# Kernel tuning notes

Hardware: AMD Instinct MI355X
Metric: run time of the kernel (lower is better)

Reference implementation:

```python
import jax, jax.numpy as jnp
import numpy as np

N = 2048      # nodes
E = 65536     # edges (avg degree 32)
D_I = 64      # input feature dim
D_O = 64      # output feature dim
EPS = 1e-6


def _one_hot_incidence(key, n, e):
    # each edge column has a single 1 at its endpoint node row -> [N, E]
    idx = jax.random.randint(key, (e,), 0, n)
    return jnp.zeros((n, e), jnp.float32).at[idx, jnp.arange(e)].set(1.0)


def setup_inputs() -> dict:
    key = jax.random.key(0)
    k_x, k_s, k_t, k_wf, k_ww = jax.random.split(key, 5)
    x = jax.random.normal(k_x, (N, D_I), jnp.float32)
    src = _one_hot_incidence(k_s, N, E)
    tgt = _one_hot_incidence(k_t, N, E)
    # xavier-uniform init for Linear(2*d_i, d_o) and Linear(2*d_i, 1)
    lim_f = float(np.sqrt(6.0 / (2 * D_I + D_O)))
    lim_w = float(np.sqrt(6.0 / (2 * D_I + 1)))
    W_f = jax.random.uniform(k_wf, (2 * D_I, D_O), jnp.float32, -lim_f, lim_f)
    b_f = jnp.zeros((D_O,), jnp.float32)
    W_w = jax.random.uniform(k_ww, (2 * D_I, 1), jnp.float32, -lim_w, lim_w)
    b_w = jnp.zeros((1,), jnp.float32)
    return {"x": x, "src": src, "tgt": tgt,
            "W_f": W_f, "b_f": b_f, "W_w": W_w, "b_w": b_w}


def reference(x, src, tgt, W_f, b_f, W_w, b_w):
    # gather source/target node features per edge via dense one-hot matmuls
    hsrc = src.T @ x                      # [E, d_i]
    htgt = tgt.T @ x                      # [E, d_i]
    h = jnp.concatenate([hsrc, htgt], axis=1)   # [E, 2*d_i]
    y = jax.nn.relu(h @ W_f + b_f)        # [E, d_o]
    a = h @ W_w + b_w                     # [E, 1]
    a_max = jnp.mean(a, axis=0, keepdims=True)
    a_exp = jnp.exp(a - a_max)            # [E, 1]
    a_sum = tgt @ a_exp                   # [N, 1] segment-sum over edges per target node
    a_tgt = tgt.T @ a_sum                 # [E, 1] broadcast denominators back to edges
    a_att = a_exp / (a_tgt + EPS)         # edge softmax weights
    o = tgt @ (y * a_att)                 # [N, d_o] weighted scatter-sum
    return o
```

## Files before the change

kernel.cpp:

```cpp
#include <hip/hip_runtime.h>
#include <hip/hip_bf16.h>

#define N_NODES 2048
#define N_EDGES 65536
#define D_IN    64
#define D_OUT   64
#define GAT_EPS 1e-6f

typedef unsigned short u16;
typedef unsigned int   u32;
typedef __attribute__((ext_vector_type(8))) short frag8;
typedef __attribute__((ext_vector_type(4))) float f32x4;

__device__ __forceinline__ u16 f2bf(float f) {
    union { u32 u; float f; } x; x.f = f;
    u32 lsb = (x.u >> 16) & 1u;
    x.u += 0x7fffu + lsb;
    return (u16)(x.u >> 16);
}

__global__ void k_extract(const uint4* __restrict__ src, const uint4* __restrict__ tgt,
                          int* __restrict__ sidx, int* __restrict__ tidx,
                          float* __restrict__ zero_base) {
    u32 b = blockIdx.x, tid = threadIdx.x;
    if (b < 520u) {
        u32 zi = b * 256u + tid;
        if (zi < 133120u) zero_base[zi] = 0.0f;
    }
    const uint4* m; int* idx;
    if (b < 2048u) { m = src; idx = sidx; }
    else           { m = tgt; idx = tidx; b -= 2048u; }
    u32 t0 = b * 256u + tid;
    const u32 S = 524288u;
    #pragma unroll 4
    for (u32 it = 0; it < 64u; ++it) {
        u32 t = t0 + it * S;
        uint4 v = m[t];
        if (v.x | v.y | v.z | v.w) {
            u32 elem = t * 4u;
            int n = (int)(elem >> 16);
            int e = (int)(elem & 65535u);
            if (v.x) idx[e]     = n;
            if (v.y) idx[e + 1] = n;
            if (v.z) idx[e + 2] = n;
            if (v.w) idx[e + 3] = n;
        }
    }
}

__global__ void __launch_bounds__(256) k_fused(
        const float* __restrict__ x,
        const int* __restrict__ sidx, const int* __restrict__ tidx,
        const float* __restrict__ Wf, const float* __restrict__ bf,
        const float* __restrict__ Ww, const float* __restrict__ bw,
        float* __restrict__ a_sum, float* __restrict__ out_acc) {
    __shared__ u16 wt[D_OUT * 2 * D_IN];
    __shared__ float ww[2 * D_IN];
    int tid = threadIdx.x;
    if (tid < 2 * D_IN) ww[tid] = Ww[tid];
    for (int i = tid; i < 2 * D_IN * D_OUT; i += 256) {
        int k = i >> 6, d = i & 63;
        wt[d * 128 + k] = f2bf(Wf[i]);
    }
    __syncthreads();

    int wave = tid >> 6, lane = tid & 63;
    int q = lane >> 4, r = lane & 15;
    int e0 = blockIdx.x * 64 + wave * 16;

    int s_r = sidx[e0 + r] & (N_NODES - 1);
    int t_r = tidx[e0 + r] & (N_NODES - 1);
    const float* xs = x + s_r * D_IN;
    const float* xt = x + t_r * D_IN;

    frag8 afr[4];
    float part = 0.0f;
    #pragma unroll
    for (int c = 0; c < 4; ++c) {
        const float* base = (c < 2 ? xs : xt) + (c & 1) * 32 + q * 8;
        int kb = (c >> 1) * 64 + (c & 1) * 32 + q * 8;
        float4 lo = *(const float4*)(base);
        float4 hi = *(const float4*)(base + 4);
        part += lo.x * ww[kb]     + lo.y * ww[kb + 1]
              + lo.z * ww[kb + 2] + lo.w * ww[kb + 3]
              + hi.x * ww[kb + 4] + hi.y * ww[kb + 5]
              + hi.z * ww[kb + 6] + hi.w * ww[kb + 7];
        frag8 f;
        f[0] = (short)f2bf(lo.x); f[1] = (short)f2bf(lo.y);
        f[2] = (short)f2bf(lo.z); f[3] = (short)f2bf(lo.w);
        f[4] = (short)f2bf(hi.x); f[5] = (short)f2bf(hi.y);
        f[6] = (short)f2bf(hi.z); f[7] = (short)f2bf(hi.w);
        afr[c] = f;
    }
    part += __shfl_xor(part, 16);
    part += __shfl_xor(part, 32);
    float ae = expf(part + bw[0]);
    if (lane < 16) atomicAdd(&a_sum[t_r], ae);

    f32x4 acc[4] = { {0,0,0,0}, {0,0,0,0}, {0,0,0,0}, {0,0,0,0} };
    #pragma unroll
    for (int c = 0; c < 4; ++c) {
        #pragma unroll
        for (int dt = 0; dt < 4; ++dt) {
            frag8 bfr = *(const frag8*)(&wt[(dt * 16 + r) * 128 + c * 32 + q * 8]);
            acc[dt] = __builtin_amdgcn_mfma_f32_16x16x32_bf16(afr[c], bfr, acc[dt], 0, 0, 0);
        }
    }

    #pragma unroll
    for (int reg = 0; reg < 4; ++reg) {
        float w  = __shfl(ae,  q * 4 + reg);
        int   tg = __shfl(t_r, q * 4 + reg);
        #pragma unroll
        for (int dt = 0; dt < 4; ++dt) {
            int d = dt * 16 + r;
            float y = acc[dt][reg] + bf[d];
            y = y > 0.0f ? y : 0.0f;
            atomicAdd(&out_acc[tg * D_OUT + d], y * w);
        }
    }
}

__global__ void k_norm(const float* __restrict__ out_acc, const float* __restrict__ a_sum,
                       float* __restrict__ out) {
    int i = blockIdx.x * 256 + threadIdx.x;
    out[i] = out_acc[i] / (a_sum[i >> 6] + GAT_EPS);
}

extern "C" void kernel_launch(void* const* d_in, const int* in_sizes, int n_in,
                              void* d_out, int out_size, void* d_ws, size_t ws_size,
                              hipStream_t stream) {
    const float* x   = (const float*)d_in[0];
    const float* src = (const float*)d_in[1];
    const float* tgt = (const float*)d_in[2];
    const float* Wf  = (const float*)d_in[3];
    const float* bf  = (const float*)d_in[4];
    const float* Ww  = (const float*)d_in[5];
    const float* bw  = (const float*)d_in[6];
    float* out = (float*)d_out;

    char* ws = (char*)d_ws;
    float* a_sum   = (float*)(ws);
    float* out_acc = (float*)(ws + 8192);
    int*   sidx    = (int*)  (ws + 8192 + 524288);
    int*   tidx    = (int*)  (ws + 532480 + 262144);

    k_extract<<<4096, 256, 0, stream>>>((const uint4*)src, (const uint4*)tgt,
                                        sidx, tidx, (float*)ws);
    k_fused<<<N_EDGES / 64, 256, 0, stream>>>(x, sidx, tidx, Wf, bf, Ww, bw,
                                              a_sum, out_acc);
    k_norm<<<(N_NODES * D_OUT) / 256, 256, 0, stream>>>(out_acc, a_sum, out);
}
```

Measured before the change: 997.0 us.

## Replace atomic scatter with per-edge buffer and per-node ballot gather

Instead of atomically adding weighted edge features and exp weights into per-node accumulators, the edge kernel now writes per-edge weighted features and exp values to a workspace buffer. A new gather kernel, one block per node, scans the whole target index array with wave ballots, sums matching edges, and normalises in place. This removes the atomics, the zeroing pass and the norm kernel. In exchange each node block rereads all 65536 target indices, and a 16 MB intermediate is written and then read back.

```diff
diff --git a/kernel.cpp b/kernel.cpp
--- a/kernel.cpp
+++ b/kernel.cpp
@@ -9,6 +9,7 @@
 
 typedef unsigned short u16;
 typedef unsigned int   u32;
+typedef unsigned long long u64;
 typedef __attribute__((ext_vector_type(8))) short frag8;
 typedef __attribute__((ext_vector_type(4))) float f32x4;
 
@@ -20,13 +21,8 @@
 }
 
 __global__ void k_extract(const uint4* __restrict__ src, const uint4* __restrict__ tgt,
-                          int* __restrict__ sidx, int* __restrict__ tidx,
-                          float* __restrict__ zero_base) {
+                          int* __restrict__ sidx, int* __restrict__ tidx) {
     u32 b = blockIdx.x, tid = threadIdx.x;
-    if (b < 520u) {
-        u32 zi = b * 256u + tid;
-        if (zi < 133120u) zero_base[zi] = 0.0f;
-    }
     const uint4* m; int* idx;
     if (b < 2048u) { m = src; idx = sidx; }
     else           { m = tgt; idx = tidx; b -= 2048u; }
@@ -48,12 +44,12 @@
     }
 }
 
-__global__ void __launch_bounds__(256) k_fused(
+__global__ void __launch_bounds__(256) k_edges(
         const float* __restrict__ x,
         const int* __restrict__ sidx, const int* __restrict__ tidx,
         const float* __restrict__ Wf, const float* __restrict__ bf,
         const float* __restrict__ Ww, const float* __restrict__ bw,
-        float* __restrict__ a_sum, float* __restrict__ out_acc) {
+        float* __restrict__ ae_out, float* __restrict__ P) {
     __shared__ u16 wt[D_OUT * 2 * D_IN];
     __shared__ float ww[2 * D_IN];
     int tid = threadIdx.x;
@@ -69,9 +65,9 @@
     int e0 = blockIdx.x * 64 + wave * 16;
 
     int s_r = sidx[e0 + r] & (N_NODES - 1);
-    int t_r = tidx[e0 + r] & (N_NODES - 1);
+    int t_r = tidx[e0 + r] & (N_NODES - 1);   (void)t_r;
     const float* xs = x + s_r * D_IN;
-    const float* xt = x + t_r * D_IN;
+    const float* xt = x + (tidx[e0 + r] & (N_NODES - 1)) * D_IN;
 
     frag8 afr[4];
     float part = 0.0f;
@@ -95,7 +91,7 @@
     part += __shfl_xor(part, 16);
     part += __shfl_xor(part, 32);
     float ae = expf(part + bw[0]);
-    if (lane < 16) atomicAdd(&a_sum[t_r], ae);
+    if (lane < 16) ae_out[e0 + r] = ae;
 
     f32x4 acc[4] = { {0,0,0,0}, {0,0,0,0}, {0,0,0,0}, {0,0,0,0} };
     #pragma unroll
@@ -109,22 +105,51 @@
 
     #pragma unroll
     for (int reg = 0; reg < 4; ++reg) {
-        float w  = __shfl(ae,  q * 4 + reg);
-        int   tg = __shfl(t_r, q * 4 + reg);
+        float w = __shfl(ae, q * 4 + reg);
+        int   e = e0 + q * 4 + reg;
         #pragma unroll
         for (int dt = 0; dt < 4; ++dt) {
             int d = dt * 16 + r;
             float y = acc[dt][reg] + bf[d];
             y = y > 0.0f ? y : 0.0f;
-            atomicAdd(&out_acc[tg * D_OUT + d], y * w);
+            P[e * D_OUT + d] = y * w;
         }
     }
 }
 
-__global__ void k_norm(const float* __restrict__ out_acc, const float* __restrict__ a_sum,
-                       float* __restrict__ out) {
-    int i = blockIdx.x * 256 + threadIdx.x;
-    out[i] = out_acc[i] / (a_sum[i >> 6] + GAT_EPS);
+__global__ void __launch_bounds__(256) k_gather(
+        const int* __restrict__ tidx, const float* __restrict__ ae,
+        const float* __restrict__ P, float* __restrict__ out) {
+    int n  = blockIdx.x;
+    int wv = threadIdx.x >> 6, l = threadIdx.x & 63;
+    const uint4* t4 = (const uint4*)tidx;
+    float acc = 0.0f, asum = 0.0f;
+    #pragma unroll 4
+    for (int it = 0; it < 64; ++it) {
+        int base = wv * 16384 + it * 256;
+        uint4 v = t4[(base >> 2) + l];
+        u32 c[4] = { v.x, v.y, v.z, v.w };
+        #pragma unroll
+        for (int j = 0; j < 4; ++j) {
+            u64 m = __ballot(c[j] == (u32)n);
+            while (m) {
+                int b = __ffsll(m) - 1; m &= m - 1;
+                int e = base + 4 * b + j;
+                asum += ae[e];
+                acc  += P[e * D_OUT + l];
+            }
+        }
+    }
+    __shared__ float red[4][D_OUT];
+    __shared__ float reds[4];
+    red[wv][l] = acc;
+    if (l == 0) reds[wv] = asum;
+    __syncthreads();
+    if (threadIdx.x < D_OUT) {
+        float tot = red[0][l] + red[1][l] + red[2][l] + red[3][l];
+        float as  = reds[0] + reds[1] + reds[2] + reds[3];
+        out[n * D_OUT + l] = tot / (as + GAT_EPS);
+    }
 }
 
 extern "C" void kernel_launch(void* const* d_in, const int* in_sizes, int n_in,
@@ -140,14 +165,14 @@
     float* out = (float*)d_out;
 
     char* ws = (char*)d_ws;
-    float* a_sum   = (float*)(ws);
-    float* out_acc = (float*)(ws + 8192);
-    int*   sidx    = (int*)  (ws + 8192 + 524288);
-    int*   tidx    = (int*)  (ws + 532480 + 262144);
+    int*   sidx = (int*)  (ws);
+    int*   tidx = (int*)  (ws + 262144);
+    float* ae   = (float*)(ws + 524288);
+    float* P    = (float*)(ws + 786432);
 
     k_extract<<<4096, 256, 0, stream>>>((const uint4*)src, (const uint4*)tgt,
-                                        sidx, tidx, (float*)ws);
-    k_fused<<<N_EDGES / 64, 256, 0, stream>>>(x, sidx, tidx, Wf, bf, Ww, bw,
-                                              a_sum, out_acc);
-    k_norm<<<(N_NODES * D_OUT) / 256, 256, 0, stream>>>(out_acc, a_sum, out);
+                                        sidx, tidx);
+    k_edges<<<N_EDGES / 64, 256, 0, stream>>>(x, sidx, tidx, Wf, bf, Ww, bw,
+                                              ae, P);
+    k_gather<<<N_NODES, 256, 0, stream>>>(tidx, ae, P, out);
 }
```

Result: no change. 1.013 ms (+1.6%).
